# Optimization experiments

Hardware: AMD Instinct MI355X
Metric: run time of the kernel (lower is better)

## Reference

```python
import jax, jax.numpy as jnp
import numpy as np

EPS = 1e-08
COS_ID_THRESH = 0.9999
L_SH, R_SH, NECK = 11, 12, 0


def setup_inputs() -> dict:
    key = jax.random.key(0)
    landmarks = jax.random.normal(key, (32768, 543, 3), dtype=jnp.float32)
    return {"landmarks": landmarks}


def reference(landmarks):
    # landmarks: (T, N, 3)
    ls = landmarks[:, L_SH]            # (T, 3)
    rs = landmarks[:, R_SH]            # (T, 3)
    neck = landmarks[:, NECK]          # (T, 3)

    sv = rs - ls                       # shoulder vector, (T, 3)
    s = jnp.linalg.norm(sv, axis=-1) + EPS          # per-frame scale, (T,)

    # project shoulder vector to xz-plane and normalize
    sxz = sv * jnp.array([1.0, 0.0, 1.0], dtype=sv.dtype)
    sxz = sxz / (jnp.linalg.norm(sxz, axis=-1, keepdims=True) + EPS)

    # cos of angle to target [1,0,0] is just the x component
    cos_t = jnp.clip(sxz[:, 0], -1.0, 1.0)          # (T,)
    sin_t = jnp.sqrt(jnp.clip(1.0 - cos_t * cos_t, 0.0, None))

    # Rodrigues for fixed axis (0,1,0): K and K@K are constants
    K = jnp.array([[0.0, 0.0, 1.0],
                   [0.0, 0.0, 0.0],
                   [-1.0, 0.0, 0.0]], dtype=landmarks.dtype)
    K2 = K @ K                                       # diag(-1, 0, -1)
    I3 = jnp.eye(3, dtype=landmarks.dtype)

    R = I3 + sin_t[:, None, None] * K + (1.0 - cos_t)[:, None, None] * K2  # (T,3,3)
    R = jnp.where((jnp.abs(cos_t) > COS_ID_THRESH)[:, None, None], I3, R)

    centered = landmarks - neck[:, None, :]          # (T, N, 3)
    # rotated[t] = centered[t] @ R[t].T
    rotated = jnp.einsum('tnj,tij->tni', centered, R)
    return rotated / s[:, None, None]
```

## Files before the change

### kernel.cpp

```cpp
#include <hip/hip_runtime.h>
#include <math.h>

#define N_LM 543
#define ROW (N_LM * 3)
#define L_SH 11
#define R_SH 12

__global__ __launch_bounds__(256)
void sim3_kernel(const float* __restrict__ in, float* __restrict__ out) {
    const int t = blockIdx.x;
    const float* __restrict__ row = in + (size_t)t * ROW;
    float* __restrict__ orow = out + (size_t)t * ROW;

    const float nx = row[0], ny = row[1], nz = row[2];
    const float lsx = row[L_SH * 3 + 0], lsy = row[L_SH * 3 + 1], lsz = row[L_SH * 3 + 2];
    const float rsx = row[R_SH * 3 + 0], rsy = row[R_SH * 3 + 1], rsz = row[R_SH * 3 + 2];

    const float svx = rsx - lsx;
    const float svy = rsy - lsy;
    const float svz = rsz - lsz;

    const float s = sqrtf(svx * svx + svy * svy + svz * svz) + 1e-8f;
    const float inv_s = 1.0f / s;

    const float sxz_n = sqrtf(svx * svx + svz * svz) + 1e-8f;
    float c = svx / sxz_n;
    c = fminf(fmaxf(c, -1.0f), 1.0f);
    float st = sqrtf(fmaxf(1.0f - c * c, 0.0f));

    if (fabsf(c) > 0.9999f) { c = 1.0f; st = 0.0f; }

    for (int n = threadIdx.x; n < N_LM; n += blockDim.x) {
        const int o = n * 3;
        const float x = row[o + 0] - nx;
        const float y = row[o + 1] - ny;
        const float z = row[o + 2] - nz;
        orow[o + 0] = (c * x + st * z) * inv_s;
        orow[o + 1] = y * inv_s;
        orow[o + 2] = (-st * x + c * z) * inv_s;
    }
}

extern "C" void kernel_launch(void* const* d_in, const int* in_sizes, int n_in,
                              void* d_out, int out_size, void* d_ws, size_t ws_size,
                              hipStream_t stream) {
    const float* in = (const float*)d_in[0];
    float* out = (float*)d_out;
    const int T = in_sizes[0] / ROW;
    sim3_kernel<<<T, 256, 0, stream>>>(in, out);
}
```

Before: 348.8 us.

## Process four rows per block with float4 vectorized loads and stores

Each block now handles four consecutive frames. A few threads compute the per-frame rotation parameters into shared memory, then all threads stream the contiguous four-row span with float4 loads and stores, deinterlacing xyz in registers. This targets the scalar stride-3 accesses and per-row block overhead of a bandwidth-bound kernel. It adds a shared-memory sync and a scalar fallback path for a partial last group.

```diff
diff --git a/kernel.cpp b/kernel.cpp
--- a/kernel.cpp
+++ b/kernel.cpp
@@ -3,41 +3,100 @@
 
 #define N_LM 543
 #define ROW (N_LM * 3)
+#define RPB 4
+#define CHUNKS (RPB * N_LM / 4)
 #define L_SH 11
 #define R_SH 12
 
 __global__ __launch_bounds__(256)
-void sim3_kernel(const float* __restrict__ in, float* __restrict__ out) {
-    const int t = blockIdx.x;
-    const float* __restrict__ row = in + (size_t)t * ROW;
-    float* __restrict__ orow = out + (size_t)t * ROW;
+void sim3_kernel(const float* __restrict__ in, float* __restrict__ out, int T) {
+    __shared__ float P[RPB][8];
+    const int b = blockIdx.x;
+    const int row0 = b * RPB;
 
-    const float nx = row[0], ny = row[1], nz = row[2];
-    const float lsx = row[L_SH * 3 + 0], lsy = row[L_SH * 3 + 1], lsz = row[L_SH * 3 + 2];
-    const float rsx = row[R_SH * 3 + 0], rsy = row[R_SH * 3 + 1], rsz = row[R_SH * 3 + 2];
+    if (threadIdx.x < RPB) {
+        const int t = row0 + threadIdx.x;
+        if (t < T) {
+            const float* __restrict__ row = in + (size_t)t * ROW;
+            const float nx = row[0], ny = row[1], nz = row[2];
+            const float lsx = row[L_SH * 3 + 0], lsy = row[L_SH * 3 + 1], lsz = row[L_SH * 3 + 2];
+            const float rsx = row[R_SH * 3 + 0], rsy = row[R_SH * 3 + 1], rsz = row[R_SH * 3 + 2];
 
-    const float svx = rsx - lsx;
-    const float svy = rsy - lsy;
-    const float svz = rsz - lsz;
+            const float svx = rsx - lsx;
+            const float svy = rsy - lsy;
+            const float svz = rsz - lsz;
 
-    const float s = sqrtf(svx * svx + svy * svy + svz * svz) + 1e-8f;
-    const float inv_s = 1.0f / s;
+            const float s = sqrtf(svx * svx + svy * svy + svz * svz) + 1e-8f;
+            const float inv_s = 1.0f / s;
 
-    const float sxz_n = sqrtf(svx * svx + svz * svz) + 1e-8f;
-    float c = svx / sxz_n;
-    c = fminf(fmaxf(c, -1.0f), 1.0f);
-    float st = sqrtf(fmaxf(1.0f - c * c, 0.0f));
+            const float sxz_n = sqrtf(svx * svx + svz * svz) + 1e-8f;
+            float c = svx / sxz_n;
+            c = fminf(fmaxf(c, -1.0f), 1.0f);
+            float st = sqrtf(fmaxf(1.0f - c * c, 0.0f));
+            if (fabsf(c) > 0.9999f) { c = 1.0f; st = 0.0f; }
 
-    if (fabsf(c) > 0.9999f) { c = 1.0f; st = 0.0f; }
+            P[threadIdx.x][0] = c;
+            P[threadIdx.x][1] = st;
+            P[threadIdx.x][2] = inv_s;
+            P[threadIdx.x][3] = nx;
+            P[threadIdx.x][4] = ny;
+            P[threadIdx.x][5] = nz;
+        }
+    }
+    __syncthreads();
 
-    for (int n = threadIdx.x; n < N_LM; n += blockDim.x) {
-        const int o = n * 3;
-        const float x = row[o + 0] - nx;
-        const float y = row[o + 1] - ny;
-        const float z = row[o + 2] - nz;
-        orow[o + 0] = (c * x + st * z) * inv_s;
-        orow[o + 1] = y * inv_s;
-        orow[o + 2] = (-st * x + c * z) * inv_s;
+    if (row0 + RPB <= T) {
+        const float4* __restrict__ src = (const float4*)(in + (size_t)row0 * ROW);
+        float4*       __restrict__ dst = (float4*)(out + (size_t)row0 * ROW);
+
+        for (int ch = threadIdx.x; ch < CHUNKS; ch += 256) {
+            const float4 v0 = src[ch * 3 + 0];
+            const float4 v1 = src[ch * 3 + 1];
+            const float4 v2 = src[ch * 3 + 2];
+
+            const float xin[4] = { v0.x, v0.w, v1.z, v2.y };
+            const float yin[4] = { v0.y, v1.x, v1.w, v2.z };
+            const float zin[4] = { v0.z, v1.y, v2.x, v2.w };
+            float o[12];
+
+            const int l0 = ch * 4;
+            #pragma unroll
+            for (int m = 0; m < 4; ++m) {
+                const int l = l0 + m;
+                const int r = (l >= N_LM) + (l >= 2 * N_LM) + (l >= 3 * N_LM);
+                const float c  = P[r][0];
+                const float st = P[r][1];
+                const float is = P[r][2];
+                const float x = xin[m] - P[r][3];
+                const float y = yin[m] - P[r][4];
+                const float z = zin[m] - P[r][5];
+                o[m * 3 + 0] = (c * x + st * z) * is;
+                o[m * 3 + 1] = y * is;
+                o[m * 3 + 2] = (c * z - st * x) * is;
+            }
+
+            dst[ch * 3 + 0] = make_float4(o[0], o[1],  o[2],  o[3]);
+            dst[ch * 3 + 1] = make_float4(o[4], o[5],  o[6],  o[7]);
+            dst[ch * 3 + 2] = make_float4(o[8], o[9],  o[10], o[11]);
+        }
+    } else {
+        for (int rr = 0; rr < RPB; ++rr) {
+            const int t = row0 + rr;
+            if (t >= T) break;
+            const float* __restrict__ row  = in  + (size_t)t * ROW;
+            float*       __restrict__ orow = out + (size_t)t * ROW;
+            const float c  = P[rr][0], st = P[rr][1], is = P[rr][2];
+            const float nx = P[rr][3], ny = P[rr][4], nz = P[rr][5];
+            for (int n = threadIdx.x; n < N_LM; n += 256) {
+                const int o = n * 3;
+                const float x = row[o + 0] - nx;
+                const float y = row[o + 1] - ny;
+                const float z = row[o + 2] - nz;
+                orow[o + 0] = (c * x + st * z) * is;
+                orow[o + 1] = y * is;
+                orow[o + 2] = (c * z - st * x) * is;
+            }
+        }
     }
 }
 
@@ -47,5 +106,6 @@
     const float* in = (const float*)d_in[0];
     float* out = (float*)d_out;
     const int T = in_sizes[0] / ROW;
-    sim3_kernel<<<T, 256, 0, stream>>>(in, out);
+    const int grid = (T + RPB - 1) / RPB;
+    sim3_kernel<<<grid, 256, 0, stream>>>(in, out, T);
 }
```

After: 356.4 us. +2.2%, slower.
